# Performance work log

Hardware: AMD Instinct MI355X
Metric: run time of the kernel (lower is better)

The kernel has to match this reference:

```python
import jax, jax.numpy as jnp
import numpy as np

VOCAB = 32000
EMB = 1024


def setup_inputs() -> dict:
    key = jax.random.key(0)
    k1, k2 = jax.random.split(key)
    tokens = jax.random.randint(k1, (8, 4096), 0, VOCAB, dtype=jnp.int64 if jax.config.jax_enable_x64 else jnp.int32)
    # nn.Linear(vocab, emb, bias=False) weight: [emb, vocab]
    W = jax.random.normal(k2, (EMB, VOCAB), dtype=jnp.float32) * (1.0 / np.sqrt(VOCAB))
    return {"tokens": tokens, "W": W}


def reference(tokens, W):
    # Original: one_hot(tokens, vocab) @ W.T  ==  gather columns of W
    # out[b, s, :] = W[:, tokens[b, s]]
    return W.T[tokens]  # [B, S, EMB]
```

## Files before the change

kernel.cpp:

```cpp
#include <hip/hip_runtime.h>

#define VOCAB 32000
#define EMB   1024
#define TPB   256
#define COLS  32
#define CH    256
#define PITCH 258
#define CAP   1024

typedef float f32x4 __attribute__((ext_vector_type(4)));

__global__ __launch_bounds__(TPB) void tok_emb_fused(
    const float* __restrict__ W, const int* __restrict__ tokens,
    f32x4* __restrict__ out4, int n_tokens) {
    __shared__ float lds[COLS * PITCH];
    __shared__ int   list[CAP];
    __shared__ int   cnt;

    const int v0  = blockIdx.x * COLS;
    const int tid = threadIdx.x;

    auto run = [&](int lo, int hi) {
        __syncthreads();
        if (tid == 0) cnt = 0;
        __syncthreads();

        const int nvec = (hi - lo) >> 2;
        for (int q = tid; q < nvec; q += TPB) {
            const int4 tk = *reinterpret_cast<const int4*>(&tokens[lo + (q << 2)]);
            const int tv[4] = {tk.x, tk.y, tk.z, tk.w};
#pragma unroll
            for (int jj = 0; jj < 4; ++jj) {
                const unsigned d = (unsigned)(tv[jj] - v0);
                if (d < COLS) {
                    const int p = atomicAdd(&cnt, 1);
                    if (p < CAP) list[p] = ((lo + (q << 2) + jj) << 5) | (int)d;
                }
            }
        }
        for (int i = lo + (nvec << 2) + tid; i < hi; i += TPB) {
            const unsigned d = (unsigned)(tokens[i] - v0);
            if (d < COLS) {
                const int p = atomicAdd(&cnt, 1);
                if (p < CAP) list[p] = (i << 5) | (int)d;
            }
        }
        __syncthreads();
        const int m = cnt < CAP ? cnt : CAP;
        if (m == 0) return;

        for (int c0 = 0; c0 < EMB; c0 += CH) {
            __syncthreads();
#pragma unroll
            for (int it = 0; it < (CH * COLS / 4) / TPB; ++it) {
                const int idx = tid + it * TPB;
                const int r   = idx >> 3;
                const int cc  = (idx & 7) << 2;
                const float4 v = *reinterpret_cast<const float4*>(
                    &W[(size_t)(c0 + r) * VOCAB + (size_t)(v0 + cc)]);
                lds[(cc + 0) * PITCH + r] = v.x;
                lds[(cc + 1) * PITCH + r] = v.y;
                lds[(cc + 2) * PITCH + r] = v.z;
                lds[(cc + 3) * PITCH + r] = v.w;
            }
            __syncthreads();

            const int total = m << 6;
            for (int j = tid; j < total; j += TPB) {
                const int mi = j >> 6, lane = j & 63;
                const int ent = list[mi];
                const int t   = ent >> 5, col = ent & 31;
                const float* rp = &lds[col * PITCH + (lane << 2)];
                const float2 a = *reinterpret_cast<const float2*>(rp);
                const float2 b = *reinterpret_cast<const float2*>(rp + 2);
                f32x4 o;
                o.x = a.x; o.y = a.y; o.z = b.x; o.w = b.y;
                __builtin_nontemporal_store(
                    o, &out4[(size_t)t * (EMB / 4) + (c0 >> 2) + lane]);
            }
        }
    };

    run(0, n_tokens);
    __syncthreads();
    if (cnt > CAP) {
        for (int lo = 0; lo < n_tokens; lo += CAP) {
            const int hi = (lo + CAP < n_tokens) ? lo + CAP : n_tokens;
            run(lo, hi);
        }
    }
}

extern "C" void kernel_launch(void* const* d_in, const int* in_sizes, int n_in,
                              void* d_out, int out_size, void* d_ws, size_t ws_size,
                              hipStream_t stream) {
    const int*   tokens   = (const int*)d_in[0];
    const float* W        = (const float*)d_in[1];
    f32x4*       out4     = (f32x4*)d_out;
    const int    n_tokens = in_sizes[0];

    tok_emb_fused<<<VOCAB / COLS, TPB, 0, stream>>>(W, tokens, out4, n_tokens);
}
```

Measured before the change: 59.31 us.

## Pre-bucket tokens by vocab tile in separate kernels instead of per-block full scans

Previously each of the 1000 blocks scanned all 32768 tokens to find the ones falling in its 32-column vocab tile. Now a zero kernel and a bucketing kernel build per-tile lists with global atomics in workspace, and the main kernel just loads its list. That removes roughly 1000x redundant token reads. The main kernel also moves to 512 threads with 128-row chunks. The cost is two extra kernel launches and global atomics, with a slow fallback when a tile overflows 256 entries or no workspace is available.

```diff
diff --git a/kernel.cpp b/kernel.cpp
--- a/kernel.cpp
+++ b/kernel.cpp
@@ -2,53 +2,62 @@
 
 #define VOCAB 32000
 #define EMB   1024
-#define TPB   256
+#define TPB   512
 #define COLS  32
-#define CH    256
-#define PITCH 258
-#define CAP   1024
+#define TILES (VOCAB / COLS)
+#define CH    128
+#define PITCH 130
+#define CAP_T 256
 
 typedef float f32x4 __attribute__((ext_vector_type(4)));
 
-__global__ __launch_bounds__(TPB) void tok_emb_fused(
+__global__ __launch_bounds__(TPB) void tok_emb_zero(int* __restrict__ cnt) {
+    const int i = blockIdx.x * TPB + threadIdx.x;
+    if (i < TILES) cnt[i] = 0;
+}
+
+__global__ __launch_bounds__(TPB) void tok_emb_bucket(
+    const int* __restrict__ tokens, int* __restrict__ cnt,
+    int* __restrict__ bucket, int n_tokens) {
+    const int i4 = (blockIdx.x * TPB + threadIdx.x) * 4;
+    if (i4 + 3 < n_tokens) {
+        const int4 tk = *reinterpret_cast<const int4*>(&tokens[i4]);
+        const int tv[4] = {tk.x, tk.y, tk.z, tk.w};
+#pragma unroll
+        for (int j = 0; j < 4; ++j) {
+            const int tok = tv[j];
+            const unsigned tile = (unsigned)tok >> 5;
+            if (tile < TILES) {
+                const int p = atomicAdd(&cnt[tile], 1);
+                if (p < CAP_T) bucket[tile * CAP_T + p] = ((i4 + j) << 5) | (tok & 31);
+            }
+        }
+    } else {
+        for (int i = i4; i < n_tokens; ++i) {
+            const int tok = tokens[i];
+            const unsigned tile = (unsigned)tok >> 5;
+            if (tile < TILES) {
+                const int p = atomicAdd(&cnt[tile], 1);
+                if (p < CAP_T) bucket[tile * CAP_T + p] = (i << 5) | (tok & 31);
+            }
+        }
+    }
+}
+
+__global__ __launch_bounds__(TPB) void tok_emb_main(
     const float* __restrict__ W, const int* __restrict__ tokens,
+    const int* __restrict__ cnt, const int* __restrict__ bucket,
     f32x4* __restrict__ out4, int n_tokens) {
     __shared__ float lds[COLS * PITCH];
-    __shared__ int   list[CAP];
-    __shared__ int   cnt;
+    __shared__ int   list[CAP_T];
+    __shared__ int   scnt;
 
-    const int v0  = blockIdx.x * COLS;
-    const int tid = threadIdx.x;
+    const int tile = blockIdx.x;
+    const int v0   = tile * COLS;
+    const int tid  = threadIdx.x;
 
-    auto run = [&](int lo, int hi) {
-        __syncthreads();
-        if (tid == 0) cnt = 0;
-        __syncthreads();
-
-        const int nvec = (hi - lo) >> 2;
-        for (int q = tid; q < nvec; q += TPB) {
-            const int4 tk = *reinterpret_cast<const int4*>(&tokens[lo + (q << 2)]);
-            const int tv[4] = {tk.x, tk.y, tk.z, tk.w};
-#pragma unroll
-            for (int jj = 0; jj < 4; ++jj) {
-                const unsigned d = (unsigned)(tv[jj] - v0);
-                if (d < COLS) {
-                    const int p = atomicAdd(&cnt, 1);
-                    if (p < CAP) list[p] = ((lo + (q << 2) + jj) << 5) | (int)d;
-                }
-            }
-        }
-        for (int i = lo + (nvec << 2) + tid; i < hi; i += TPB) {
-            const unsigned d = (unsigned)(tokens[i] - v0);
-            if (d < COLS) {
-                const int p = atomicAdd(&cnt, 1);
-                if (p < CAP) list[p] = (i << 5) | (int)d;
-            }
-        }
-        __syncthreads();
-        const int m = cnt < CAP ? cnt : CAP;
+    auto process = [&](int m) {
         if (m == 0) return;
-
         for (int c0 = 0; c0 < EMB; c0 += CH) {
             __syncthreads();
 #pragma unroll
@@ -65,9 +74,9 @@
             }
             __syncthreads();
 
-            const int total = m << 6;
+            const int total = m << 5;
             for (int j = tid; j < total; j += TPB) {
-                const int mi = j >> 6, lane = j & 63;
+                const int mi = j >> 5, lane = j & 31;
                 const int ent = list[mi];
                 const int t   = ent >> 5, col = ent & 31;
                 const float* rp = &lds[col * PITCH + (lane << 2)];
@@ -81,12 +90,26 @@
         }
     };
 
-    run(0, n_tokens);
-    __syncthreads();
-    if (cnt > CAP) {
-        for (int lo = 0; lo < n_tokens; lo += CAP) {
-            const int hi = (lo + CAP < n_tokens) ? lo + CAP : n_tokens;
-            run(lo, hi);
+    const int m_total = (bucket != nullptr) ? cnt[tile] : CAP_T + 1;
+    if (m_total <= CAP_T) {
+        for (int j = tid; j < m_total; j += TPB) list[j] = bucket[tile * CAP_T + j];
+        __syncthreads();
+        process(m_total);
+    } else {
+        for (int lo = 0; lo < n_tokens; lo += CAP_T) {
+            const int hi = (lo + CAP_T < n_tokens) ? lo + CAP_T : n_tokens;
+            __syncthreads();
+            if (tid == 0) scnt = 0;
+            __syncthreads();
+            for (int i = lo + tid; i < hi; i += TPB) {
+                const unsigned d = (unsigned)(tokens[i] - v0);
+                if (d < COLS) {
+                    const int p = atomicAdd(&scnt, 1);
+                    list[p] = (i << 5) | (int)d;
+                }
+            }
+            __syncthreads();
+            process(scnt);
         }
     }
 }
@@ -99,5 +122,17 @@
     f32x4*       out4     = (f32x4*)d_out;
     const int    n_tokens = in_sizes[0];
 
-    tok_emb_fused<<<VOCAB / COLS, TPB, 0, stream>>>(W, tokens, out4, n_tokens);
+    const size_t need = (size_t)TILES * sizeof(int)
+                      + (size_t)TILES * CAP_T * sizeof(int);
+    if (ws_size >= need) {
+        int* cnt    = (int*)d_ws;
+        int* bucket = cnt + TILES;
+        tok_emb_zero<<<(TILES + TPB - 1) / TPB, TPB, 0, stream>>>(cnt);
+        const int quads = (n_tokens + 3) / 4;
+        tok_emb_bucket<<<(quads + TPB - 1) / TPB, TPB, 0, stream>>>(
+            tokens, cnt, bucket, n_tokens);
+        tok_emb_main<<<TILES, TPB, 0, stream>>>(W, tokens, cnt, bucket, out4, n_tokens);
+    } else {
+        tok_emb_main<<<TILES, TPB, 0, stream>>>(W, tokens, nullptr, nullptr, out4, n_tokens);
+    }
 }
```

After: 61.58 us. 3.8% more time.
